# Optimization experiments

Measured on AMD Instinct MI355X. Metric: run time of the kernel, lower is better.

The kernel has to match this reference:

```python
import jax, jax.numpy as jnp
import numpy as np
import math

B, C, H, W = 8, 256, 64, 64
KEYDIM, VALDIM = 128, 256


def conv3x3(x, w, b):
    # x: [B,C,H,W], w: [O,C,3,3] -> [B,O,H,W], SAME padding (padding=1)
    y = jax.lax.conv_general_dilated(x, w, window_strides=(1, 1), padding='SAME',
                                     dimension_numbers=('NCHW', 'OIHW', 'NCHW'))
    return y + b[None, :, None, None]


def setup_inputs() -> dict:
    key = jax.random.key(0)
    ks = jax.random.split(key, 5)
    x = jax.random.normal(ks[0], (B, C, H, W), dtype=jnp.float32)
    fan_in = C * 9
    s = 1.0 / np.sqrt(fan_in)
    key_w = jax.random.uniform(ks[1], (KEYDIM, C, 3, 3), jnp.float32, -s, s)
    key_b = jax.random.uniform(ks[2], (KEYDIM,), jnp.float32, -s, s)
    val_w = jax.random.uniform(ks[3], (VALDIM, C, 3, 3), jnp.float32, -s, s)
    val_b = jax.random.uniform(ks[4], (VALDIM,), jnp.float32, -s, s)
    return {"x": x, "key_w": key_w, "key_b": key_b, "val_w": val_w, "val_b": val_b}


def reference(x, key_w, key_b, val_w, val_b):
    b_, c_, h_, w_ = x.shape
    k = conv3x3(x, key_w, key_b).reshape(b_, KEYDIM, h_ * w_)   # [B,K,N]
    v = conv3x3(x, val_w, val_b)                                 # [B,V,H,W]
    sq = jnp.sum(k * k, axis=1)                                  # [B,N]
    a = sq[:, :, None]                                           # [B,N,1]
    c2 = sq[:, None, :]                                          # [B,1,N]
    dots = 2.0 * jnp.einsum('bki,bkj->bij', k, k)                # [B,N,N]
    affinity = (-a + dots - c2) / math.sqrt(KEYDIM)              # -||ki-kj||^2 / sqrt(K)
    affinity = jax.nn.softmax(affinity, axis=1)                  # softmax over dim=1 (rows)
    self_attn = jnp.einsum('bvi,bij->bvj', v.reshape(b_, VALDIM, h_ * w_), affinity)
    self_attn = self_attn.reshape(b_, VALDIM, h_, w_)
    return jnp.concatenate((v, self_attn), axis=1)               # [B,2V,H,W]
```

## Files before the change

### kernel.cpp

```cpp
#include <hip/hip_runtime.h>
#include <hip/hip_bf16.h>
#include <cstdint>

constexpr int Bb = 8, Cc = 256, Hh = 64, Ww = 64, Nn = 4096;
constexpr int KD = 128, VD = 256, HP = 66;

typedef __attribute__((ext_vector_type(8))) short short8_t;
typedef __attribute__((ext_vector_type(4))) short shortx4;
typedef __attribute__((ext_vector_type(4))) float floatx4;

constexpr float kScale = 0.08838834764831845f * 1.4426950408889634f;
constexpr float kTwoK  = 2.0f * kScale;

static __device__ __forceinline__ ushort f2bf(float f) {
    union { float f; uint32_t u; } v{f};
    uint32_t r = v.u + 0x7FFFu + ((v.u >> 16) & 1u);
    return (ushort)(r >> 16);
}
static __device__ __forceinline__ float bf2f(ushort b) {
    union { uint32_t u; float f; } v{(uint32_t)b << 16};
    return v.f;
}
static __device__ __forceinline__ uint32_t pk_bf16(float a, float b) {
    uint32_t r;
    asm("v_cvt_pk_bf16_f32 %0, %1, %2" : "=v"(r) : "v"(a), "v"(b));
    return r;
}
static __device__ __forceinline__ float exp2_raw(float x) {
    float r;
    asm("v_exp_f32 %0, %1" : "=v"(r) : "v"(x));
    return r;
}

static __device__ __forceinline__ void gload_lds16(const void* g, void* l) {
    __builtin_amdgcn_global_load_lds((const __attribute__((address_space(1))) uint32_t*)g,
                                     (__attribute__((address_space(3))) uint32_t*)l, 16, 0, 0);
}

__global__ __launch_bounds__(256) void pad_transpose(const float* __restrict__ x,
                                                     ushort* __restrict__ xpad) {
    int bid = blockIdx.x;
    int b = bid & 7, rest = bid >> 3;
    int y = rest & 63, cg = rest >> 6;
    int t = threadIdx.x;
    __shared__ float tile[64][65];
    int xcol = t & 63;
    int crow = t >> 6;
    const float* xb = x + ((size_t)(b * Cc + cg * 64) * Nn) + y * 64;
#pragma unroll
    for (int i = 0; i < 16; i++) {
        int c = crow + i * 4;
        tile[c][xcol] = xb[(size_t)c * Nn + xcol];
    }
    __syncthreads();
    int c = t & 63;
    int x4 = t >> 6;
    ushort* dst = xpad + (((size_t)(b * HP + (y + 1)) * HP) + 1) * Cc + cg * 64 + c;
#pragma unroll
    for (int i = 0; i < 16; i++) {
        int xx = x4 + i * 4;
        dst[(size_t)xx * Cc] = f2bf(tile[c][xx]);
    }
}

__global__ __launch_bounds__(256) void repack_w(const float* __restrict__ kw,
                                                const float* __restrict__ vw,
                                                ushort* __restrict__ wtk,
                                                ushort* __restrict__ wtv) {
    int idx = blockIdx.x * 256 + threadIdx.x;
    const int nk = KD * Cc;
    const int nv = VD * Cc;
    if (idx < nk) {
        const float* src = kw + (size_t)idx * 9;
        int oc = idx / Cc, c = idx % Cc;
#pragma unroll
        for (int r = 0; r < 9; r++) wtk[((size_t)r * KD + oc) * Cc + c] = f2bf(src[r]);
    } else if (idx < nk + nv) {
        int j = idx - nk;
        const float* src = vw + (size_t)j * 9;
        int oc = j / Cc, c = j % Cc;
#pragma unroll
        for (int r = 0; r < 9; r++) wtv[((size_t)r * VD + oc) * Cc + c] = f2bf(src[r]);
    }
}

__global__ __launch_bounds__(256) void conv_k(const ushort* __restrict__ xpad,
                                              const ushort* __restrict__ wt,
                                              const float* __restrict__ bias,
                                              ushort* __restrict__ kt_out,
                                              float* __restrict__ sq_out) {
    int bid = blockIdx.x;
    int b = bid & 7, y = bid >> 3;
    int lane = threadIdx.x & 63, wv = threadIdx.x >> 6;
    int l15 = lane & 15, g = lane >> 4;
    const int swzA = l15 & 7;

    __shared__ ushort wslab[2][128 * 128];

    size_t wsoff[8];
    int ldsrow[8];
#pragma unroll
    for (int h = 0; h < 8; h++) {
        int row = wv * 32 + h * 4 + (lane >> 4);
        wsoff[h] = (size_t)row * Cc + (((lane & 15) ^ (row & 7)) * 8);
        ldsrow[h] = (wv * 32 + h * 4) * 128;
    }

    floatx4 acc[8];
#pragma unroll
    for (int m = 0; m < 8; m++) acc[m] = (floatx4){0.f, 0.f, 0.f, 0.f};

    const ushort* xb = xpad + ((size_t)b * HP * HP) * Cc;
    int xcol = wv * 16 + l15;

    auto stage = [&](int hs, int bi) {
        int r = hs >> 1, hc = hs & 1;
        const ushort* wb = wt + ((size_t)r * KD) * Cc + hc * 128;
#pragma unroll
        for (int h = 0; h < 8; h++)
            gload_lds16(wb + wsoff[h], &wslab[bi][ldsrow[h]]);
    };

    stage(0, 0);
    __syncthreads();

#pragma unroll 1
    for (int hs = 0; hs < 18; ++hs) {
        int bi = hs & 1;
        if (hs < 17) stage(hs + 1, bi ^ 1);

        int r = hs >> 1, hc = hs & 1;
        int dy = r / 3, dx = r % 3;
        const ushort* bsrc = xb + ((size_t)(y + dy) * HP + xcol + dx) * Cc + hc * 128 + g * 8;
#pragma unroll
        for (int cc = 0; cc < 4; cc++) {
            short8_t bfrag = *(const short8_t*)(bsrc + cc * 32);
#pragma unroll
            for (int m = 0; m < 8; m++) {
                short8_t afrag = *(const short8_t*)&wslab[bi][(m * 16 + l15) * 128 + ((cc * 4 + g) ^ swzA) * 8];
                acc[m] = __builtin_amdgcn_mfma_f32_16x16x32_bf16(afrag, bfrag, acc[m], 0, 0, 0);
            }
        }
        __syncthreads();
    }

    int pos = y * 64 + xcol;
    ushort* kt = kt_out + ((size_t)(b * Nn + pos)) * KD;
    float ssum = 0.f;
#pragma unroll
    for (int m = 0; m < 8; m++) {
        floatx4 bv = *(const floatx4*)(bias + m * 16 + g * 4);
        shortx4 pk;
#pragma unroll
        for (int r = 0; r < 4; r++) {
            pk[r] = (short)f2bf(acc[m][r] + bv[r]);
            float q = bf2f((ushort)pk[r]);
            ssum += q * q;
        }
        *(shortx4*)(kt + m * 16 + g * 4) = pk;
    }
    ssum += __shfl_xor(ssum, 16, 64);
    ssum += __shfl_xor(ssum, 32, 64);
    if (g == 0) sq_out[b * Nn + pos] = ssum * kScale;
}

__global__ __launch_bounds__(256) void conv_v(const ushort* __restrict__ xpad,
                                              const ushort* __restrict__ wt,
                                              const float* __restrict__ bias,
                                              float* __restrict__ f32_out,
                                              ushort* __restrict__ vb_out) {
    int bid = blockIdx.x;
    int b = bid & 7;
    int ocg = (bid >> 3) & 1;
    int y0 = (bid >> 4) * 2;
    int lane = threadIdx.x & 63, wv = threadIdx.x >> 6;
    int l15 = lane & 15, g = lane >> 4;
    int oc0 = ocg * 128;
    const int swzA = l15 & 7;

    __shared__ ushort wslab[2][128 * 128];

    size_t wsoff[8];
    int ldsrow[8];
#pragma unroll
    for (int h = 0; h < 8; h++) {
        int row = wv * 32 + h * 4 + (lane >> 4);
        wsoff[h] = (size_t)row * Cc + (((lane & 15) ^ (row & 7)) * 8);
        ldsrow[h] = (wv * 32 + h * 4) * 128;
    }

    floatx4 acc[8][2];
#pragma unroll
    for (int m = 0; m < 8; m++)
#pragma unroll
        for (int rr = 0; rr < 2; rr++) acc[m][rr] = (floatx4){0.f, 0.f, 0.f, 0.f};

    const ushort* xb = xpad + ((size_t)b * HP * HP) * Cc;
    int xcol = wv * 16 + l15;

    auto stage = [&](int hs, int bi) {
        int r = hs >> 1, hc = hs & 1;
        const ushort* wb = wt + ((size_t)r * VD + oc0) * Cc + hc * 128;
#pragma unroll
        for (int h = 0; h < 8; h++)
            gload_lds16(wb + wsoff[h], &wslab[bi][ldsrow[h]]);
    };

    stage(0, 0);
    __syncthreads();

#pragma unroll 1
    for (int hs = 0; hs < 18; ++hs) {
        int bi = hs & 1;
        if (hs < 17) stage(hs + 1, bi ^ 1);

        int r = hs >> 1, hc = hs & 1;
        int dy = r / 3, dx = r % 3;
        const ushort* bsrc0 = xb + ((size_t)(y0 + dy) * HP + xcol + dx) * Cc + hc * 128 + g * 8;
        const ushort* bsrc1 = bsrc0 + (size_t)HP * Cc;
#pragma unroll
        for (int cc = 0; cc < 4; cc++) {
            short8_t bfragA = *(const short8_t*)(bsrc0 + cc * 32);
            short8_t bfragB = *(const short8_t*)(bsrc1 + cc * 32);
#pragma unroll
            for (int m = 0; m < 8; m++) {
                short8_t afrag = *(const short8_t*)&wslab[bi][(m * 16 + l15) * 128 + ((cc * 4 + g) ^ swzA) * 8];
                acc[m][0] = __builtin_amdgcn_mfma_f32_16x16x32_bf16(afrag, bfragA, acc[m][0], 0, 0, 0);
                acc[m][1] = __builtin_amdgcn_mfma_f32_16x16x32_bf16(afrag, bfragB, acc[m][1], 0, 0, 0);
            }
        }
        __syncthreads();
    }

#pragma unroll
    for (int rr = 0; rr < 2; rr++) {
        int pos = (y0 + rr) * 64 + xcol;
#pragma unroll
        for (int m = 0; m < 8; m++) {
            floatx4 bv = *(const floatx4*)(bias + oc0 + m * 16 + g * 4);
#pragma unroll
            for (int r = 0; r < 4; r++) {
                int oc = oc0 + m * 16 + g * 4 + r;
                float v = acc[m][rr][r] + bv[r];
                f32_out[((size_t)(b * 512 + oc)) * Nn + pos] = v;
                vb_out[((size_t)(b * VD + oc)) * Nn + pos] = f2bf(v);
            }
        }
    }
}

__global__ __launch_bounds__(256, 3) void attn_kernel(const ushort* __restrict__ kt,
                                                      const ushort* __restrict__ vb,
                                                      const float* __restrict__ sq2,
                                                      float* __restrict__ out) {
    int bid = blockIdx.x;
    int b = bid & 7, jt = bid >> 3;
    int lane = threadIdx.x & 63, wv = threadIdx.x >> 6;
    int l15 = lane & 15, g = lane >> 4;

    __shared__ ushort bufK[64 * 128];
    __shared__ ushort bufV[256 * 64];

    const ushort* ktb = kt + ((size_t)b * Nn) * KD;
    const ushort* vbb = vb + ((size_t)b * VD) * Nn;
    const float* sqb = sq2 + b * Nn;

    const ushort* skp[4];
#pragma unroll
    for (int h = 0; h < 4; h++) {
        int sub = lane >> 4;
        int pr = h * 4 + sub;
        int ilog = ((wv & 1) << 5) + (h << 3) + ((wv >> 1) << 2) + sub;
        skp[h] = ktb + (size_t)ilog * KD + ((l15 ^ (pr & 7)) * 8);
    }
    const ushort* svp[8];
#pragma unroll
    for (int h = 0; h < 8; h++) {
        int vd = wv * 64 + h * 8 + (lane >> 3);
        svp[h] = vbb + (size_t)vd * Nn + (((lane & 7) ^ (vd & 7)) * 8);
    }

    int j = jt * 64 + wv * 16 + l15;
    short8_t kj[4];
#pragma unroll
    for (int kk = 0; kk < 4; kk++)
        kj[kk] = *(const short8_t*)(ktb + (size_t)j * KD + kk * 32 + g * 8);

    floatx4 acc[16];
#pragma unroll
    for (int m = 0; m < 16; m++) acc[m] = (floatx4){0.f, 0.f, 0.f, 0.f};
    float dsum = 0.f;
    const int swzA = l15 & 7;

#pragma unroll
    for (int h = 0; h < 4; h++) gload_lds16(skp[h], &bufK[(wv * 16 + h * 4) * 128]);
#pragma unroll
    for (int h = 0; h < 8; h++) gload_lds16(svp[h], &bufV[(wv * 64 + h * 8) * 64]);
    __syncthreads();

#pragma unroll 1
    for (int it = 0; it < 64; ++it) {
        int i0 = it * 64;

        floatx4 sacc[4];
#pragma unroll
        for (int f = 0; f < 4; f++) sacc[f] = (floatx4){0.f, 0.f, 0.f, 0.f};
#pragma unroll
        for (int kk = 0; kk < 4; kk++) {
#pragma unroll
            for (int f = 0; f < 4; f++) {
                short8_t afr = *(const short8_t*)&bufK[(f * 16 + l15) * 128 + ((kk * 4 + g) ^ swzA) * 8];
                sacc[f] = __builtin_amdgcn_mfma_f32_16x16x32_bf16(afr, kj[kk], sacc[f], 0, 0, 0);
            }
        }
        __syncthreads();

        if (it < 63) {
#pragma unroll
            for (int h = 0; h < 4; h++)
                gload_lds16(skp[h] + (size_t)(i0 + 64) * KD, &bufK[(wv * 16 + h * 4) * 128]);
        }

        uint32_t w2[4][2];
#pragma unroll
        for (int f = 0; f < 4; f++) {
            floatx4 sqi = *(const floatx4*)(sqb + i0 + ((f & 1) << 5) + (g << 3) + ((f >> 1) << 2));
            float p0 = exp2_raw(sacc[f][0] * kTwoK - sqi[0]);
            float p1 = exp2_raw(sacc[f][1] * kTwoK - sqi[1]);
            float p2 = exp2_raw(sacc[f][2] * kTwoK - sqi[2]);
            float p3 = exp2_raw(sacc[f][3] * kTwoK - sqi[3]);
            dsum += (p0 + p1) + (p2 + p3);
            w2[f][0] = pk_bf16(p0, p1);
            w2[f][1] = pk_bf16(p2, p3);
        }

#pragma unroll
        for (int k2 = 0; k2 < 2; k2++) {
            union { uint32_t u[4]; short8_t s; } pu;
            pu.u[0] = w2[k2][0];
            pu.u[1] = w2[k2][1];
            pu.u[2] = w2[k2 | 2][0];
            pu.u[3] = w2[k2 | 2][1];
            short8_t pfr = pu.s;
#pragma unroll
            for (int m = 0; m < 16; m++) {
                short8_t vfr = *(const short8_t*)&bufV[(m * 16 + l15) * 64 + ((k2 * 4 + g) ^ swzA) * 8];
                acc[m] = __builtin_amdgcn_mfma_f32_16x16x32_bf16(vfr, pfr, acc[m], 0, 0, 0);
            }
        }
        __syncthreads();

        if (it < 63) {
#pragma unroll
            for (int h = 0; h < 8; h++)
                gload_lds16(svp[h] + (i0 + 64), &bufV[(wv * 64 + h * 8) * 64]);
        }
    }

    dsum += __shfl_xor(dsum, 16, 64);
    dsum += __shfl_xor(dsum, 32, 64);
    float rden = 1.f / dsum;

    float* ob = out + ((size_t)(b * 512 + 256)) * Nn + j;
#pragma unroll
    for (int m = 0; m < 16; m++) {
#pragma unroll
        for (int r = 0; r < 4; r++) {
            int vd = m * 16 + g * 4 + r;
            ob[(size_t)vd * Nn] = acc[m][r] * rden;
        }
    }
}

extern "C" void kernel_launch(void* const* d_in, const int* in_sizes, int n_in,
                              void* d_out, int out_size, void* d_ws, size_t ws_size,
                              hipStream_t stream) {
    const float* x     = (const float*)d_in[0];
    const float* kw    = (const float*)d_in[1];
    const float* kbias = (const float*)d_in[2];
    const float* vw    = (const float*)d_in[3];
    const float* vbias = (const float*)d_in[4];
    float* out = (float*)d_out;
    char* ws = (char*)d_ws;

    constexpr size_t XPAD = 0;
    constexpr size_t WTK  = 17842176;
    constexpr size_t WTV  = 18432000;
    constexpr size_t KT   = 19611648;
    constexpr size_t VB   = 28000256;
    constexpr size_t SQ   = 44777472;

    ushort* xpad = (ushort*)(ws + XPAD);
    ushort* wtk  = (ushort*)(ws + WTK);
    ushort* wtv  = (ushort*)(ws + WTV);
    ushort* ktw  = (ushort*)(ws + KT);
    ushort* vbw  = (ushort*)(ws + VB);
    float*  sqw  = (float*)(ws + SQ);

    hipMemsetAsync(xpad, 0, 17842176, stream);
    pad_transpose<<<dim3(2048), 256, 0, stream>>>(x, xpad);
    repack_w<<<dim3(384), 256, 0, stream>>>(kw, vw, wtk, wtv);
    conv_k<<<dim3(512), 256, 0, stream>>>(xpad, wtk, kbias, ktw, sqw);
    conv_v<<<dim3(512), 256, 0, stream>>>(xpad, wtv, vbias, out, vbw);
    attn_kernel<<<dim3(512), 256, 0, stream>>>(ktw, vbw, sqw, out);
}
```

Before: 258.0 us.

## Merge key/value convs into one launch, zero pad borders in-kernel, prioritize MFMA

Replaces the full-buffer memset of the padded input with border-only zeroing inside pad_transpose, removing a roughly 17 MB write pass. Merges the separate key and value convolution kernels into one 1024-block launch that dispatches on block index, which removes a launch and lets both convs share the GPU. Adds s_setprio around the MFMA sections of the attention kernel to favour matrix issue across waves. The fused kernel carries the larger register footprint of the value branch, which may lower occupancy for key blocks.

```diff
diff --git a/kernel.cpp b/kernel.cpp
--- a/kernel.cpp
+++ b/kernel.cpp
@@ -52,6 +52,28 @@
         int c = crow + i * 4;
         tile[c][xcol] = xb[(size_t)c * Nn + xcol];
     }
+
+    ushort* xbb = xpad + ((size_t)b * HP * HP) * Cc + cg * 64;
+    if (y == 0) {
+        for (int idx = t; idx < HP * 64; idx += 256) {
+            int xx = idx >> 6, c = idx & 63;
+            xbb[(size_t)xx * Cc + c] = 0;
+        }
+    }
+    if (y == 63) {
+        for (int idx = t; idx < HP * 64; idx += 256) {
+            int xx = idx >> 6, c = idx & 63;
+            xbb[((size_t)65 * HP + xx) * Cc + c] = 0;
+        }
+    }
+    {
+        int c = t & 63, which = t >> 6;
+        if (which < 2) {
+            int xx = which * 65;
+            xbb[((size_t)(y + 1) * HP + xx) * Cc + c] = 0;
+        }
+    }
+
     __syncthreads();
     int c = t & 63;
     int x4 = t >> 6;
@@ -84,13 +106,16 @@
     }
 }
 
-__global__ __launch_bounds__(256) void conv_k(const ushort* __restrict__ xpad,
-                                              const ushort* __restrict__ wt,
-                                              const float* __restrict__ bias,
-                                              ushort* __restrict__ kt_out,
-                                              float* __restrict__ sq_out) {
+__global__ __launch_bounds__(256) void conv_kv(const ushort* __restrict__ xpad,
+                                               const ushort* __restrict__ wtv,
+                                               const ushort* __restrict__ wtk,
+                                               const float* __restrict__ vbias,
+                                               const float* __restrict__ kbias,
+                                               float* __restrict__ f32_out,
+                                               ushort* __restrict__ vb_out,
+                                               ushort* __restrict__ kt_out,
+                                               float* __restrict__ sq_out) {
     int bid = blockIdx.x;
-    int b = bid & 7, y = bid >> 3;
     int lane = threadIdx.x & 63, wv = threadIdx.x >> 6;
     int l15 = lane & 15, g = lane >> 4;
     const int swzA = l15 & 7;
@@ -106,146 +131,126 @@
         ldsrow[h] = (wv * 32 + h * 4) * 128;
     }
 
-    floatx4 acc[8];
-#pragma unroll
-    for (int m = 0; m < 8; m++) acc[m] = (floatx4){0.f, 0.f, 0.f, 0.f};
-
-    const ushort* xb = xpad + ((size_t)b * HP * HP) * Cc;
     int xcol = wv * 16 + l15;
 
-    auto stage = [&](int hs, int bi) {
-        int r = hs >> 1, hc = hs & 1;
-        const ushort* wb = wt + ((size_t)r * KD) * Cc + hc * 128;
-#pragma unroll
-        for (int h = 0; h < 8; h++)
-            gload_lds16(wb + wsoff[h], &wslab[bi][ldsrow[h]]);
-    };
-
-    stage(0, 0);
-    __syncthreads();
+    if (bid < 512) {
+        int b = bid & 7;
+        int ocg = (bid >> 3) & 1;
+        int y0 = (bid >> 4) * 2;
+        int oc0 = ocg * 128;
+        const ushort* xb = xpad + ((size_t)b * HP * HP) * Cc;
+
+        floatx4 acc[8][2];
+#pragma unroll
+        for (int m = 0; m < 8; m++)
+#pragma unroll
+            for (int rr = 0; rr < 2; rr++) acc[m][rr] = (floatx4){0.f, 0.f, 0.f, 0.f};
+
+        auto stage = [&](int hs, int bi) {
+            int r = hs >> 1, hc = hs & 1;
+            const ushort* wb = wtv + ((size_t)r * VD + oc0) * Cc + hc * 128;
+#pragma unroll
+            for (int h = 0; h < 8; h++)
+                gload_lds16(wb + wsoff[h], &wslab[bi][ldsrow[h]]);
+        };
+
+        stage(0, 0);
+        __syncthreads();
 
 #pragma unroll 1
-    for (int hs = 0; hs < 18; ++hs) {
-        int bi = hs & 1;
-        if (hs < 17) stage(hs + 1, bi ^ 1);
-
-        int r = hs >> 1, hc = hs & 1;
-        int dy = r / 3, dx = r % 3;
-        const ushort* bsrc = xb + ((size_t)(y + dy) * HP + xcol + dx) * Cc + hc * 128 + g * 8;
-#pragma unroll
-        for (int cc = 0; cc < 4; cc++) {
-            short8_t bfrag = *(const short8_t*)(bsrc + cc * 32);
+        for (int hs = 0; hs < 18; ++hs) {
+            int bi = hs & 1;
+            if (hs < 17) stage(hs + 1, bi ^ 1);
+            int r = hs >> 1, hc = hs & 1;
+            int dy = r / 3, dx = r % 3;
+            const ushort* bsrc0 = xb + ((size_t)(y0 + dy) * HP + xcol + dx) * Cc + hc * 128 + g * 8;
+            const ushort* bsrc1 = bsrc0 + (size_t)HP * Cc;
+#pragma unroll
+            for (int cc = 0; cc < 4; cc++) {
+                short8_t bfragA = *(const short8_t*)(bsrc0 + cc * 32);
+                short8_t bfragB = *(const short8_t*)(bsrc1 + cc * 32);
+#pragma unroll
+                for (int m = 0; m < 8; m++) {
+                    short8_t afrag = *(const short8_t*)&wslab[bi][(m * 16 + l15) * 128 + ((cc * 4 + g) ^ swzA) * 8];
+                    acc[m][0] = __builtin_amdgcn_mfma_f32_16x16x32_bf16(afrag, bfragA, acc[m][0], 0, 0, 0);
+                    acc[m][1] = __builtin_amdgcn_mfma_f32_16x16x32_bf16(afrag, bfragB, acc[m][1], 0, 0, 0);
+                }
+            }
+            __syncthreads();
+        }
+
+#pragma unroll
+        for (int rr = 0; rr < 2; rr++) {
+            int pos = (y0 + rr) * 64 + xcol;
 #pragma unroll
             for (int m = 0; m < 8; m++) {
-                short8_t afrag = *(const short8_t*)&wslab[bi][(m * 16 + l15) * 128 + ((cc * 4 + g) ^ swzA) * 8];
-                acc[m] = __builtin_amdgcn_mfma_f32_16x16x32_bf16(afrag, bfrag, acc[m], 0, 0, 0);
-            }
-        }
+                floatx4 bv = *(const floatx4*)(vbias + oc0 + m * 16 + g * 4);
+#pragma unroll
+                for (int r = 0; r < 4; r++) {
+                    int oc = oc0 + m * 16 + g * 4 + r;
+                    float v = acc[m][rr][r] + bv[r];
+                    f32_out[((size_t)(b * 512 + oc)) * Nn + pos] = v;
+                    vb_out[((size_t)(b * VD + oc)) * Nn + pos] = f2bf(v);
+                }
+            }
+        }
+    } else {
+        int bid2 = bid - 512;
+        int b = bid2 & 7, y = bid2 >> 3;
+        const ushort* xb = xpad + ((size_t)b * HP * HP) * Cc;
+
+        floatx4 acc[8];
+#pragma unroll
+        for (int m = 0; m < 8; m++) acc[m] = (floatx4){0.f, 0.f, 0.f, 0.f};
+
+        auto stage = [&](int hs, int bi) {
+            int r = hs >> 1, hc = hs & 1;
+            const ushort* wb = wtk + ((size_t)r * KD) * Cc + hc * 128;
+#pragma unroll
+            for (int h = 0; h < 8; h++)
+                gload_lds16(wb + wsoff[h], &wslab[bi][ldsrow[h]]);
+        };
+
+        stage(0, 0);
         __syncthreads();
-    }
-
-    int pos = y * 64 + xcol;
-    ushort* kt = kt_out + ((size_t)(b * Nn + pos)) * KD;
-    float ssum = 0.f;
-#pragma unroll
-    for (int m = 0; m < 8; m++) {
-        floatx4 bv = *(const floatx4*)(bias + m * 16 + g * 4);
-        shortx4 pk;
-#pragma unroll
-        for (int r = 0; r < 4; r++) {
-            pk[r] = (short)f2bf(acc[m][r] + bv[r]);
-            float q = bf2f((ushort)pk[r]);
-            ssum += q * q;
-        }
-        *(shortx4*)(kt + m * 16 + g * 4) = pk;
-    }
-    ssum += __shfl_xor(ssum, 16, 64);
-    ssum += __shfl_xor(ssum, 32, 64);
-    if (g == 0) sq_out[b * Nn + pos] = ssum * kScale;
-}
-
-__global__ __launch_bounds__(256) void conv_v(const ushort* __restrict__ xpad,
-                                              const ushort* __restrict__ wt,
-                                              const float* __restrict__ bias,
-                                              float* __restrict__ f32_out,
-                                              ushort* __restrict__ vb_out) {
-    int bid = blockIdx.x;
-    int b = bid & 7;
-    int ocg = (bid >> 3) & 1;
-    int y0 = (bid >> 4) * 2;
-    int lane = threadIdx.x & 63, wv = threadIdx.x >> 6;
-    int l15 = lane & 15, g = lane >> 4;
-    int oc0 = ocg * 128;
-    const int swzA = l15 & 7;
-
-    __shared__ ushort wslab[2][128 * 128];
-
-    size_t wsoff[8];
-    int ldsrow[8];
-#pragma unroll
-    for (int h = 0; h < 8; h++) {
-        int row = wv * 32 + h * 4 + (lane >> 4);
-        wsoff[h] = (size_t)row * Cc + (((lane & 15) ^ (row & 7)) * 8);
-        ldsrow[h] = (wv * 32 + h * 4) * 128;
-    }
-
-    floatx4 acc[8][2];
-#pragma unroll
-    for (int m = 0; m < 8; m++)
-#pragma unroll
-        for (int rr = 0; rr < 2; rr++) acc[m][rr] = (floatx4){0.f, 0.f, 0.f, 0.f};
-
-    const ushort* xb = xpad + ((size_t)b * HP * HP) * Cc;
-    int xcol = wv * 16 + l15;
-
-    auto stage = [&](int hs, int bi) {
-        int r = hs >> 1, hc = hs & 1;
-        const ushort* wb = wt + ((size_t)r * VD + oc0) * Cc + hc * 128;
-#pragma unroll
-        for (int h = 0; h < 8; h++)
-            gload_lds16(wb + wsoff[h], &wslab[bi][ldsrow[h]]);
-    };
-
-    stage(0, 0);
-    __syncthreads();
 
 #pragma unroll 1
-    for (int hs = 0; hs < 18; ++hs) {
-        int bi = hs & 1;
-        if (hs < 17) stage(hs + 1, bi ^ 1);
-
-        int r = hs >> 1, hc = hs & 1;
-        int dy = r / 3, dx = r % 3;
-        const ushort* bsrc0 = xb + ((size_t)(y0 + dy) * HP + xcol + dx) * Cc + hc * 128 + g * 8;
-        const ushort* bsrc1 = bsrc0 + (size_t)HP * Cc;
-#pragma unroll
-        for (int cc = 0; cc < 4; cc++) {
-            short8_t bfragA = *(const short8_t*)(bsrc0 + cc * 32);
-            short8_t bfragB = *(const short8_t*)(bsrc1 + cc * 32);
-#pragma unroll
-            for (int m = 0; m < 8; m++) {
-                short8_t afrag = *(const short8_t*)&wslab[bi][(m * 16 + l15) * 128 + ((cc * 4 + g) ^ swzA) * 8];
-                acc[m][0] = __builtin_amdgcn_mfma_f32_16x16x32_bf16(afrag, bfragA, acc[m][0], 0, 0, 0);
-                acc[m][1] = __builtin_amdgcn_mfma_f32_16x16x32_bf16(afrag, bfragB, acc[m][1], 0, 0, 0);
-            }
-        }
-        __syncthreads();
-    }
-
-#pragma unroll
-    for (int rr = 0; rr < 2; rr++) {
-        int pos = (y0 + rr) * 64 + xcol;
+        for (int hs = 0; hs < 18; ++hs) {
+            int bi = hs & 1;
+            if (hs < 17) stage(hs + 1, bi ^ 1);
+            int r = hs >> 1, hc = hs & 1;
+            int dy = r / 3, dx = r % 3;
+            const ushort* bsrc = xb + ((size_t)(y + dy) * HP + xcol + dx) * Cc + hc * 128 + g * 8;
+#pragma unroll
+            for (int cc = 0; cc < 4; cc++) {
+                short8_t bfrag = *(const short8_t*)(bsrc + cc * 32);
+#pragma unroll
+                for (int m = 0; m < 8; m++) {
+                    short8_t afrag = *(const short8_t*)&wslab[bi][(m * 16 + l15) * 128 + ((cc * 4 + g) ^ swzA) * 8];
+                    acc[m] = __builtin_amdgcn_mfma_f32_16x16x32_bf16(afrag, bfrag, acc[m], 0, 0, 0);
+                }
+            }
+            __syncthreads();
+        }
+
+        int pos = y * 64 + xcol;
+        ushort* kt = kt_out + ((size_t)(b * Nn + pos)) * KD;
+        float ssum = 0.f;
 #pragma unroll
         for (int m = 0; m < 8; m++) {
-            floatx4 bv = *(const floatx4*)(bias + oc0 + m * 16 + g * 4);
+            floatx4 bv = *(const floatx4*)(kbias + m * 16 + g * 4);
+            shortx4 pk;
 #pragma unroll
             for (int r = 0; r < 4; r++) {
-                int oc = oc0 + m * 16 + g * 4 + r;
-                float v = acc[m][rr][r] + bv[r];
-                f32_out[((size_t)(b * 512 + oc)) * Nn + pos] = v;
-                vb_out[((size_t)(b * VD + oc)) * Nn + pos] = f2bf(v);
-            }
-        }
+                pk[r] = (short)f2bf(acc[m][r] + bv[r]);
+                float q = bf2f((ushort)pk[r]);
+                ssum += q * q;
+            }
+            *(shortx4*)(kt + m * 16 + g * 4) = pk;
+        }
+        ssum += __shfl_xor(ssum, 16, 64);
+        ssum += __shfl_xor(ssum, 32, 64);
+        if (g == 0) sq_out[b * Nn + pos] = ssum * kScale;
     }
 }
 
@@ -305,6 +310,7 @@
         floatx4 sacc[4];
 #pragma unroll
         for (int f = 0; f < 4; f++) sacc[f] = (floatx4){0.f, 0.f, 0.f, 0.f};
+        __builtin_amdgcn_s_setprio(1);
 #pragma unroll
         for (int kk = 0; kk < 4; kk++) {
 #pragma unroll
@@ -313,6 +319,7 @@
                 sacc[f] = __builtin_amdgcn_mfma_f32_16x16x32_bf16(afr, kj[kk], sacc[f], 0, 0, 0);
             }
         }
+        __builtin_amdgcn_s_setprio(0);
         __syncthreads();
 
         if (it < 63) {
@@ -334,6 +341,7 @@
             w2[f][1] = pk_bf16(p2, p3);
         }
 
+        __builtin_amdgcn_s_setprio(1);
 #pragma unroll
         for (int k2 = 0; k2 < 2; k2++) {
             union { uint32_t u[4]; short8_t s; } pu;
@@ -348,6 +356,7 @@
                 acc[m] = __builtin_amdgcn_mfma_f32_16x16x32_bf16(vfr, pfr, acc[m], 0, 0, 0);
             }
         }
+        __builtin_amdgcn_s_setprio(0);
         __syncthreads();
 
         if (it < 63) {
@@ -397,10 +406,9 @@
     ushort* vbw  = (ushort*)(ws + VB);
     float*  sqw  = (float*)(ws + SQ);
 
-    hipMemsetAsync(xpad, 0, 17842176, stream);
     pad_transpose<<<dim3(2048), 256, 0, stream>>>(x, xpad);
     repack_w<<<dim3(384), 256, 0, stream>>>(kw, vw, wtk, wtv);
-    conv_k<<<dim3(512), 256, 0, stream>>>(xpad, wtk, kbias, ktw, sqw);
-    conv_v<<<dim3(512), 256, 0, stream>>>(xpad, wtv, vbias, out, vbw);
+    conv_kv<<<dim3(1024), 256, 0, stream>>>(xpad, wtv, wtk, vbias, kbias,
+                                            out, vbw, ktw, sqw);
     attn_kernel<<<dim3(512), 256, 0, stream>>>(ktw, vbw, sqw, out);
 }
```

After: 259.4 us. No clear change (+0.6%).
